# Optimization experiments

Hardware: AMD Instinct MI355X
Metric: run time of the kernel (lower is better)

The kernel has to match this reference:

```python
import jax, jax.numpy as jnp
import numpy as np

DIM = 1024          # config.dim
HID = 1024          # config.expert_hidden, already multiple of 64
N_EXP = 8           # num_routed_experts
TOP_K = 2           # top_k_experts
N_LOOPS = 4         # recursive_loops
B, S = 4, 1024


def setup_inputs() -> dict:
    key = jax.random.key(0)
    ks = jax.random.split(key, 10)
    def init(k, shape, fan_in):
        return jax.random.normal(k, shape, jnp.float32) * (fan_in ** -0.5)
    return {
        "x": jax.random.normal(ks[0], (B, S, DIM), jnp.float32),
        # shared expert (stored as [in, out] so forward is x @ W)
        "sg": init(ks[1], (DIM, HID), DIM),
        "su": init(ks[2], (DIM, HID), DIM),
        "sd": init(ks[3], (HID, DIM), HID),
        # routed experts stacked: [E, in, out]
        "Wg": init(ks[4], (N_EXP, DIM, HID), DIM),
        "Wu": init(ks[5], (N_EXP, DIM, HID), DIM),
        "Wd": init(ks[6], (N_EXP, HID, DIM), HID),
        # router: Linear(2*dim -> E, bias=False), stored [2*dim, E]
        "Wr": init(ks[7], (2 * DIM, N_EXP), 2 * DIM),
        # loop embedding table [num_loops, dim]
        "loop_table": jax.random.normal(ks[8], (N_LOOPS, DIM), jnp.float32),
        "loop_idx": 1,
    }


def _swiglu(x, wg, wu, wd):
    return (jax.nn.silu(x @ wg) * (x @ wu)) @ wd


def reference(x, sg, su, sd, Wg, Wu, Wd, Wr, loop_table, loop_idx):
    b, s, d = x.shape
    n = b * s
    xf = x.reshape(n, d)

    # shared expert (always active)
    shared = _swiglu(xf, sg, su, sd)  # [n, d]

    # loop-aware router: concat(x, loop_emb) @ Wr
    loop_emb = loop_table[loop_idx]                               # [d]
    router_in = jnp.concatenate(
        [xf, jnp.broadcast_to(loop_emb, (n, d))], axis=-1)        # [n, 2d]
    logits = router_in @ Wr                                       # [n, E]
    probs = jax.nn.sigmoid(logits)
    topw, topi = jax.lax.top_k(probs, TOP_K)                      # [n, k]

    # combine weights: combine[n, e] = sum_k topw[n,k] * (topi[n,k]==e)
    combine = jnp.zeros((n, N_EXP), x.dtype).at[
        jnp.arange(n)[:, None], topi].add(topw)                   # [n, E]

    # per-expert SwiGLU, combined with routing weights.
    # (dense-over-experts formulation; math identical to sort/dispatch/scatter)
    gate = jnp.einsum('nd,edh->neh', xf, Wg)                      # [n, E, H]
    up = jnp.einsum('nd,edh->neh', xf, Wu)                        # [n, E, H]
    h = jax.nn.silu(gate) * up                                    # [n, E, H]
    routed = jnp.einsum('neh,ehd,ne->nd', h, Wd, combine)         # [n, d]

    return (shared + routed).reshape(b, s, d)
```

## Files before the change

kernel.cpp:

```cpp
#include <hip/hip_runtime.h>
#include <cstdint>
#include <cstddef>

typedef __attribute__((ext_vector_type(8))) short short8;
typedef __attribute__((ext_vector_type(4))) float floatx4;

#define NTOK   4096
#define SHBASE 8192
#define NSLOT  12288
#define MAT_ELEMS (1024 * 1024)

__device__ __forceinline__ unsigned short f2b(float f) {
  unsigned u = __float_as_uint(f);
  u = (u + 0x7fffu + ((u >> 16) & 1u)) >> 16;
  return (unsigned short)u;
}

#define GLD16(gsrc, ldst)                                                              \
  __builtin_amdgcn_global_load_lds(                                                    \
      (const __attribute__((address_space(1))) unsigned int*)(gsrc),                   \
      (__attribute__((address_space(3))) unsigned int*)(ldst), 16, 0, 0)

__global__ void setup_kernel(const float* __restrict__ Wr,
                             const float* __restrict__ loopTable,
                             const int* __restrict__ loopIdx,
                             float* __restrict__ bias, int* __restrict__ cnt) {
  int t = threadIdx.x;
  if (t < 9) cnt[t] = (t == 8) ? NTOK : 0;
  if (t < 8) bias[t] = 0.0f;
  __syncthreads();
  const float* emb = loopTable + (size_t)(*loopIdx) * 1024;
  float partial[8] = {0, 0, 0, 0, 0, 0, 0, 0};
  for (int d = t; d < 1024; d += 256) {
    float ev = emb[d];
    const float* wr = Wr + (size_t)(1024 + d) * 8;
#pragma unroll
    for (int e = 0; e < 8; e++) partial[e] += ev * wr[e];
  }
#pragma unroll
  for (int off = 32; off > 0; off >>= 1)
#pragma unroll
    for (int e = 0; e < 8; e++) partial[e] += __shfl_xor(partial[e], off, 64);
  if ((t & 63) == 0)
#pragma unroll
    for (int e = 0; e < 8; e++) atomicAdd(&bias[e], partial[e]);
}

__global__ __launch_bounds__(256) void router_kernel(
    const float* __restrict__ x, const float* __restrict__ Wr,
    const float* __restrict__ bias, unsigned short* __restrict__ packedX,
    int* __restrict__ cnt, int* __restrict__ permSparse,
    float* __restrict__ wSparse, int* __restrict__ permToken,
    float* __restrict__ slotW) {
  int tid = threadIdx.x;
  int lane = tid & 63;
  int seg = __builtin_amdgcn_readfirstlane(tid >> 6);
  int tok0 = blockIdx.x << 6;
  int tok = tok0 + lane;

  __shared__ float red[4][64][9];
  __shared__ int lcnt[8];
  __shared__ int lbase[8];
  __shared__ int sE[64][2];
  __shared__ float sP[64][2];
  __shared__ int sPos[64][2];

  if (tid < 8) lcnt[tid] = 0;

  float lg[8] = {0, 0, 0, 0, 0, 0, 0, 0};
  const float* xr = x + (size_t)tok * 1024 + seg * 256;
  const float* wr = Wr + (size_t)seg * 256 * 8;
  for (int i = 0; i < 256; i += 4) {
    float4 xv = *(const float4*)(xr + i);
    float xs[4] = {xv.x, xv.y, xv.z, xv.w};
#pragma unroll
    for (int r = 0; r < 4; r++) {
      const float4* w4 = (const float4*)(wr + (size_t)(i + r) * 8);
      float4 wa = w4[0], wb = w4[1];
      float xv1 = xs[r];
      lg[0] += xv1 * wa.x; lg[1] += xv1 * wa.y; lg[2] += xv1 * wa.z; lg[3] += xv1 * wa.w;
      lg[4] += xv1 * wb.x; lg[5] += xv1 * wb.y; lg[6] += xv1 * wb.z; lg[7] += xv1 * wb.w;
    }
  }
#pragma unroll
  for (int e = 0; e < 8; e++) red[seg][lane][e] = lg[e];
  __syncthreads();

  if (tid < 64) {
    float l[8];
#pragma unroll
    for (int e = 0; e < 8; e++)
      l[e] = red[0][tid][e] + red[1][tid][e] + red[2][tid][e] + red[3][tid][e] + bias[e];
    int i0 = 0; float l0 = l[0];
#pragma unroll
    for (int e = 1; e < 8; e++) if (l[e] > l0) { l0 = l[e]; i0 = e; }
    int i1 = -1; float l1 = -1e30f;
#pragma unroll
    for (int e = 0; e < 8; e++) if (e != i0 && l[e] > l1) { l1 = l[e]; i1 = e; }
    float p0 = 1.0f / (1.0f + __expf(-l0));
    float p1 = 1.0f / (1.0f + __expf(-l1));
    sE[tid][0] = i0; sP[tid][0] = p0; sPos[tid][0] = atomicAdd(&lcnt[i0], 1);
    sE[tid][1] = i1; sP[tid][1] = p1; sPos[tid][1] = atomicAdd(&lcnt[i1], 1);
    int t = tok0 + tid;
    permToken[SHBASE + t] = t;
    slotW[SHBASE + t] = 1.0f;
  }
  __syncthreads();
  if (tid < 8) lbase[tid] = atomicAdd(&cnt[tid], lcnt[tid]);
  __syncthreads();
  if (tid < 64) {
    int t = tok0 + tid;
#pragma unroll
    for (int j = 0; j < 2; j++) {
      int e = sE[tid][j];
      int pos = lbase[e] + sPos[tid][j];
      permSparse[e * NTOK + pos] = t;
      wSparse[e * NTOK + pos] = sP[tid][j];
    }
  }

  const float4* xs4 = (const float4*)(x + (size_t)tok0 * 1024);
  uint2* dst = (uint2*)(packedX + (size_t)(SHBASE + tok0) * 1024);
  for (int i = tid; i < 64 * 256; i += 256) {
    float4 v = xs4[i];
    uint2 pk;
    pk.x = (unsigned)f2b(v.x) | ((unsigned)f2b(v.y) << 16);
    pk.y = (unsigned)f2b(v.z) | ((unsigned)f2b(v.w) << 16);
    dst[i] = pk;
  }
}

__global__ void scan_kernel(const int* __restrict__ cnt, int* __restrict__ offs) {
  if (threadIdx.x == 0) {
    int s = 0;
    for (int e = 0; e < 9; e++) { offs[e] = s; s += cnt[e]; }
  }
}

__global__ __launch_bounds__(256) void gather_kernel(
    const int* __restrict__ cnt, const int* __restrict__ offs,
    const int* __restrict__ permSparse, const float* __restrict__ wSparse,
    unsigned short* __restrict__ packedX, int* __restrict__ permToken,
    float* __restrict__ slotW) {
  int e = blockIdx.y;
  int r = (blockIdx.x << 2) + (threadIdx.x >> 6);
  int lane = threadIdx.x & 63;
  if (r >= cnt[e]) return;
  int token = permSparse[e * NTOK + r];
  int slot = offs[e] + r;
  if (lane == 0) { permToken[slot] = token; slotW[slot] = wSparse[e * NTOK + r]; }
  const uint4* s = (const uint4*)(packedX + (size_t)(SHBASE + token) * 1024) + lane * 2;
  uint4* d = (uint4*)(packedX + (size_t)slot * 1024) + lane * 2;
  uint4 a = s[0], b = s[1];
  d[0] = a; d[1] = b;
}

__global__ __launch_bounds__(256) void transpose_cast(
    const float* __restrict__ Wg, const float* __restrict__ Wu,
    const float* __restrict__ Wd, const float* __restrict__ sg,
    const float* __restrict__ su, const float* __restrict__ sd,
    unsigned short* __restrict__ Wt) {
  int m = blockIdx.z;
  int type = m / 9, e = m % 9;
  const float* src;
  if (type == 0)      src = (e < 8) ? Wg + (size_t)e * MAT_ELEMS : sg;
  else if (type == 1) src = (e < 8) ? Wu + (size_t)e * MAT_ELEMS : su;
  else                src = (e < 8) ? Wd + (size_t)e * MAT_ELEMS : sd;
  __shared__ float t[64][65];
  int bn = blockIdx.x << 6;
  int bk = blockIdx.y << 6;
  int tid = threadIdx.x;
  int ln = tid & 63, lk = tid >> 6;
#pragma unroll
  for (int i = 0; i < 16; i++) {
    int k = lk + (i << 2);
    t[k][ln] = src[(size_t)(bk + k) * 1024 + bn + ln];
  }
  __syncthreads();
  int wn = tid >> 4;
  int wk = (tid & 15) << 2;
  unsigned short* dstm = Wt + (size_t)m * MAT_ELEMS;
#pragma unroll
  for (int j = 0; j < 4; j++) {
    int n = wn + (j << 4);
    uint2 pk;
    pk.x = (unsigned)f2b(t[wk + 0][n]) | ((unsigned)f2b(t[wk + 1][n]) << 16);
    pk.y = (unsigned)f2b(t[wk + 2][n]) | ((unsigned)f2b(t[wk + 3][n]) << 16);
    *(uint2*)&dstm[(size_t)(bn + n) * 1024 + bk + wk] = pk;
  }
}

__global__ __launch_bounds__(256, 2) void gateup_gemm(
    const unsigned short* __restrict__ packedX, const unsigned short* __restrict__ Wt,
    const int* __restrict__ cnt, const int* __restrict__ offs,
    const float* __restrict__ slotW, unsigned short* __restrict__ Hbuf) {
  int e = blockIdx.z;
  int c = cnt[e];
  int m0 = blockIdx.y << 7;
  if (m0 >= c) return;
  int row_base = offs[e] + m0;
  int valid_m = c - m0; if (valid_m > 128) valid_m = 128;
  int n0 = blockIdx.x << 7;

  __shared__ unsigned short sA[128 * 64];
  __shared__ unsigned short sG[128 * 64];
  __shared__ unsigned short sU[128 * 64];

  int tid = threadIdx.x;
  int wv = tid >> 6, lane = tid & 63;
  int wm = wv >> 1, wn = wv & 1;

  const unsigned short* Ag = packedX + (size_t)row_base * 1024;
  const unsigned short* Gg = Wt + (size_t)e * MAT_ELEMS + (size_t)n0 * 1024;
  const unsigned short* Ug = Wt + (size_t)(9 + e) * MAT_ELEMS + (size_t)n0 * 1024;

  int srow = lane >> 3, schunk = lane & 7;

  floatx4 accG[4][4], accU[4][4];
#pragma unroll
  for (int i = 0; i < 4; i++)
#pragma unroll
    for (int j = 0; j < 4; j++) {
      accG[i][j] = floatx4{0.f, 0.f, 0.f, 0.f};
      accU[i][j] = floatx4{0.f, 0.f, 0.f, 0.f};
    }

  for (int kk = 0; kk < 1024; kk += 64) {
    __syncthreads();
#pragma unroll
    for (int j = 0; j < 4; j++) {
      int rb = (wv << 5) + (j << 3);
      size_t go = (size_t)(rb + srow) * 1024 + kk + (schunk << 3);
      GLD16(Ag + go, &sA[rb * 64]);
      GLD16(Gg + go, &sG[rb * 64]);
      GLD16(Ug + go, &sU[rb * 64]);
    }
    __syncthreads();
#pragma unroll
    for (int k0 = 0; k0 < 64; k0 += 32) {
      int aoff = ((lane >> 4) << 3) + k0;
      int arow = (wm << 6) + (lane & 15);
      short8 af[4];
#pragma unroll
      for (int mi = 0; mi < 4; mi++)
        af[mi] = *(const short8*)&sA[(arow + (mi << 4)) * 64 + aoff];
      int brow = (wn << 6) + (lane & 15);
#pragma unroll
      for (int ni = 0; ni < 4; ni++) {
        short8 gf = *(const short8*)&sG[(brow + (ni << 4)) * 64 + aoff];
        short8 uf = *(const short8*)&sU[(brow + (ni << 4)) * 64 + aoff];
#pragma unroll
        for (int mi = 0; mi < 4; mi++) {
          accG[mi][ni] = __builtin_amdgcn_mfma_f32_16x16x32_bf16(af[mi], gf, accG[mi][ni], 0, 0, 0);
          accU[mi][ni] = __builtin_amdgcn_mfma_f32_16x16x32_bf16(af[mi], uf, accU[mi][ni], 0, 0, 0);
        }
      }
    }
  }

  int colLane = lane & 15, quad = lane >> 4;
#pragma unroll
  for (int mi = 0; mi < 4; mi++) {
#pragma unroll
    for (int reg = 0; reg < 4; reg++) {
      int mrow = (wm << 6) + (mi << 4) + (quad << 2) + reg;
      if (mrow < valid_m) {
        int slot = row_base + mrow;
        float w = slotW[slot];
        unsigned short* hr = Hbuf + (size_t)slot * 1024 + n0 + (wn << 6) + colLane;
#pragma unroll
        for (int ni = 0; ni < 4; ni++) {
          float g = accG[mi][ni][reg];
          float u = accU[mi][ni][reg];
          float h = (g / (1.0f + __expf(-g))) * u * w;
          hr[ni << 4] = f2b(h);
        }
      }
    }
  }
}

template <bool ATOMIC>
__global__ __launch_bounds__(256, 2) void down_gemm(
    const unsigned short* __restrict__ Hbuf, const unsigned short* __restrict__ Wt,
    const int* __restrict__ cnt, const int* __restrict__ offs,
    const int* __restrict__ permToken, float* __restrict__ out, int e_base) {
  int e = e_base + blockIdx.z;
  int c = cnt[e];
  int m0 = blockIdx.y << 7;
  if (m0 >= c) return;
  int row_base = offs[e] + m0;
  int valid_m = c - m0; if (valid_m > 128) valid_m = 128;
  int n0 = blockIdx.x << 7;

  __shared__ unsigned short sA[128 * 64];
  __shared__ unsigned short sB[128 * 64];

  int tid = threadIdx.x;
  int wv = tid >> 6, lane = tid & 63;
  int wm = wv >> 1, wn = wv & 1;

  const unsigned short* Ag = Hbuf + (size_t)row_base * 1024;
  const unsigned short* Bg = Wt + (size_t)(18 + e) * MAT_ELEMS + (size_t)n0 * 1024;

  int srow = lane >> 3, schunk = lane & 7;

  floatx4 acc[4][4];
#pragma unroll
  for (int i = 0; i < 4; i++)
#pragma unroll
    for (int j = 0; j < 4; j++) acc[i][j] = floatx4{0.f, 0.f, 0.f, 0.f};

  for (int kk = 0; kk < 1024; kk += 64) {
    __syncthreads();
#pragma unroll
    for (int j = 0; j < 4; j++) {
      int rb = (wv << 5) + (j << 3);
      size_t go = (size_t)(rb + srow) * 1024 + kk + (schunk << 3);
      GLD16(Ag + go, &sA[rb * 64]);
      GLD16(Bg + go, &sB[rb * 64]);
    }
    __syncthreads();
#pragma unroll
    for (int k0 = 0; k0 < 64; k0 += 32) {
      int aoff = ((lane >> 4) << 3) + k0;
      int arow = (wm << 6) + (lane & 15);
      short8 af[4];
#pragma unroll
      for (int mi = 0; mi < 4; mi++)
        af[mi] = *(const short8*)&sA[(arow + (mi << 4)) * 64 + aoff];
      int brow = (wn << 6) + (lane & 15);
#pragma unroll
      for (int ni = 0; ni < 4; ni++) {
        short8 bf = *(const short8*)&sB[(brow + (ni << 4)) * 64 + aoff];
#pragma unroll
        for (int mi = 0; mi < 4; mi++)
          acc[mi][ni] = __builtin_amdgcn_mfma_f32_16x16x32_bf16(af[mi], bf, acc[mi][ni], 0, 0, 0);
      }
    }
  }

  int colLane = lane & 15, quad = lane >> 4;
#pragma unroll
  for (int mi = 0; mi < 4; mi++) {
#pragma unroll
    for (int reg = 0; reg < 4; reg++) {
      int mrow = (wm << 6) + (mi << 4) + (quad << 2) + reg;
      if (mrow < valid_m) {
        int slot = row_base + mrow;
        int token = permToken[slot];
        float* orow = out + (size_t)token * 1024 + n0 + (wn << 6) + colLane;
#pragma unroll
        for (int ni = 0; ni < 4; ni++) {
          float vvv = acc[mi][ni][reg];
          if (ATOMIC) atomicAdd(&orow[ni << 4], vvv);
          else        orow[ni << 4] = vvv;
        }
      }
    }
  }
}

extern "C" void kernel_launch(void* const* d_in, const int* in_sizes, int n_in,
                              void* d_out, int out_size, void* d_ws, size_t ws_size,
                              hipStream_t stream) {
  const float* x  = (const float*)d_in[0];
  const float* sg = (const float*)d_in[1];
  const float* su = (const float*)d_in[2];
  const float* sd = (const float*)d_in[3];
  const float* Wg = (const float*)d_in[4];
  const float* Wu = (const float*)d_in[5];
  const float* Wd = (const float*)d_in[6];
  const float* Wr = (const float*)d_in[7];
  const float* loopTable = (const float*)d_in[8];
  const int*   loopIdx   = (const int*)d_in[9];
  float* out = (float*)d_out;

  char* w = (char*)d_ws;
  unsigned short* Wt = (unsigned short*)w;       w += (size_t)27 * MAT_ELEMS * 2;
  unsigned short* packedX = (unsigned short*)w;  w += (size_t)NSLOT * 1024 * 2;
  unsigned short* Hbuf = (unsigned short*)w;     w += (size_t)NSLOT * 1024 * 2;
  int*   cnt        = (int*)w;   w += 16 * 4;
  int*   offs       = (int*)w;   w += 16 * 4;
  float* bias       = (float*)w; w += 16 * 4;
  int*   permSparse = (int*)w;   w += (size_t)8 * NTOK * 4;
  float* wSparse    = (float*)w; w += (size_t)8 * NTOK * 4;
  int*   permToken  = (int*)w;   w += (size_t)NSLOT * 4;
  float* slotW      = (float*)w; w += (size_t)NSLOT * 4;

  setup_kernel<<<1, 256, 0, stream>>>(Wr, loopTable, loopIdx, bias, cnt);
  router_kernel<<<64, 256, 0, stream>>>(x, Wr, bias, packedX, cnt, permSparse,
                                        wSparse, permToken, slotW);
  scan_kernel<<<1, 64, 0, stream>>>(cnt, offs);
  gather_kernel<<<dim3(1024, 8), 256, 0, stream>>>(cnt, offs, permSparse, wSparse,
                                                   packedX, permToken, slotW);
  transpose_cast<<<dim3(16, 16, 27), 256, 0, stream>>>(Wg, Wu, Wd, sg, su, sd, Wt);
  gateup_gemm<<<dim3(8, 32, 9), 256, 0, stream>>>(packedX, Wt, cnt, offs, slotW, Hbuf);
  down_gemm<false><<<dim3(8, 32, 1), 256, 0, stream>>>(Hbuf, Wt, cnt, offs, permToken, out, 8);
  down_gemm<true><<<dim3(8, 32, 8), 256, 0, stream>>>(Hbuf, Wt, cnt, offs, permToken, out, 0);
}
```

Measured before the change: 357.3 us.

## Gather token rows inside gate/up GEMM, swizzle LDS tiles, raise occupancy

The separate gather kernel that copied each routed token's bf16 row into a packed per-expert buffer is removed. The gate/up GEMM now loads A rows straight from the shared-token bf16 buffer through permToken indices, and a small finalize kernel only writes permToken and slotW. Both GEMMs also apply an XOR swizzle to the 16-byte chunk positions in LDS to cut bank conflicts on the MFMA fragment reads, and launch bounds go from 2 to 3 blocks per CU. The changes remove a full activation copy pass, but the indirect loads are less contiguous and the tighter register budget could cause spills.

```diff
diff --git a/kernel.cpp b/kernel.cpp
--- a/kernel.cpp
+++ b/kernel.cpp
@@ -137,22 +137,17 @@
   }
 }
 
-__global__ __launch_bounds__(256) void gather_kernel(
+__global__ __launch_bounds__(256) void finalize_kernel(
     const int* __restrict__ cnt, const int* __restrict__ offs,
     const int* __restrict__ permSparse, const float* __restrict__ wSparse,
-    unsigned short* __restrict__ packedX, int* __restrict__ permToken,
-    float* __restrict__ slotW) {
-  int e = blockIdx.y;
-  int r = (blockIdx.x << 2) + (threadIdx.x >> 6);
-  int lane = threadIdx.x & 63;
-  if (r >= cnt[e]) return;
-  int token = permSparse[e * NTOK + r];
-  int slot = offs[e] + r;
-  if (lane == 0) { permToken[slot] = token; slotW[slot] = wSparse[e * NTOK + r]; }
-  const uint4* s = (const uint4*)(packedX + (size_t)(SHBASE + token) * 1024) + lane * 2;
-  uint4* d = (uint4*)(packedX + (size_t)slot * 1024) + lane * 2;
-  uint4 a = s[0], b = s[1];
-  d[0] = a; d[1] = b;
+    int* __restrict__ permToken, float* __restrict__ slotW) {
+  int idx = blockIdx.x * 256 + threadIdx.x;
+  int e = idx >> 12, r = idx & (NTOK - 1);
+  if (e < 8 && r < cnt[e]) {
+    int slot = offs[e] + r;
+    permToken[slot] = permSparse[e * NTOK + r];
+    slotW[slot] = wSparse[e * NTOK + r];
+  }
 }
 
 __global__ __launch_bounds__(256) void transpose_cast(
@@ -190,10 +185,11 @@
   }
 }
 
-__global__ __launch_bounds__(256, 2) void gateup_gemm(
-    const unsigned short* __restrict__ packedX, const unsigned short* __restrict__ Wt,
+__global__ __launch_bounds__(256, 3) void gateup_gemm(
+    const unsigned short* __restrict__ Xb, const unsigned short* __restrict__ Wt,
     const int* __restrict__ cnt, const int* __restrict__ offs,
-    const float* __restrict__ slotW, unsigned short* __restrict__ Hbuf) {
+    const int* __restrict__ permToken, const float* __restrict__ slotW,
+    unsigned short* __restrict__ Hbuf) {
   int e = blockIdx.z;
   int c = cnt[e];
   int m0 = blockIdx.y << 7;
@@ -210,11 +206,16 @@
   int wv = tid >> 6, lane = tid & 63;
   int wm = wv >> 1, wn = wv & 1;
 
-  const unsigned short* Ag = packedX + (size_t)row_base * 1024;
   const unsigned short* Gg = Wt + (size_t)e * MAT_ELEMS + (size_t)n0 * 1024;
   const unsigned short* Ug = Wt + (size_t)(9 + e) * MAT_ELEMS + (size_t)n0 * 1024;
 
   int srow = lane >> 3, schunk = lane & 7;
+  int swc = (schunk ^ srow) << 3;
+
+  int myTok[4];
+#pragma unroll
+  for (int j = 0; j < 4; j++)
+    myTok[j] = permToken[row_base + (wv << 5) + (j << 3) + srow];
 
   floatx4 accG[4][4], accU[4][4];
 #pragma unroll
@@ -230,25 +231,25 @@
 #pragma unroll
     for (int j = 0; j < 4; j++) {
       int rb = (wv << 5) + (j << 3);
-      size_t go = (size_t)(rb + srow) * 1024 + kk + (schunk << 3);
-      GLD16(Ag + go, &sA[rb * 64]);
-      GLD16(Gg + go, &sG[rb * 64]);
-      GLD16(Ug + go, &sU[rb * 64]);
+      size_t gw = (size_t)(rb + srow) * 1024 + kk + swc;
+      GLD16(Xb + (size_t)myTok[j] * 1024 + kk + swc, &sA[rb * 64]);
+      GLD16(Gg + gw, &sG[rb * 64]);
+      GLD16(Ug + gw, &sU[rb * 64]);
     }
     __syncthreads();
 #pragma unroll
     for (int k0 = 0; k0 < 64; k0 += 32) {
-      int aoff = ((lane >> 4) << 3) + k0;
+      int swoff = (((lane >> 4) + (k0 >> 3)) ^ (lane & 7)) << 3;
       int arow = (wm << 6) + (lane & 15);
       short8 af[4];
 #pragma unroll
       for (int mi = 0; mi < 4; mi++)
-        af[mi] = *(const short8*)&sA[(arow + (mi << 4)) * 64 + aoff];
+        af[mi] = *(const short8*)&sA[(arow + (mi << 4)) * 64 + swoff];
       int brow = (wn << 6) + (lane & 15);
 #pragma unroll
       for (int ni = 0; ni < 4; ni++) {
-        short8 gf = *(const short8*)&sG[(brow + (ni << 4)) * 64 + aoff];
-        short8 uf = *(const short8*)&sU[(brow + (ni << 4)) * 64 + aoff];
+        short8 gf = *(const short8*)&sG[(brow + (ni << 4)) * 64 + swoff];
+        short8 uf = *(const short8*)&sU[(brow + (ni << 4)) * 64 + swoff];
 #pragma unroll
         for (int mi = 0; mi < 4; mi++) {
           accG[mi][ni] = __builtin_amdgcn_mfma_f32_16x16x32_bf16(af[mi], gf, accG[mi][ni], 0, 0, 0);
@@ -281,7 +282,7 @@
 }
 
 template <bool ATOMIC>
-__global__ __launch_bounds__(256, 2) void down_gemm(
+__global__ __launch_bounds__(256, 3) void down_gemm(
     const unsigned short* __restrict__ Hbuf, const unsigned short* __restrict__ Wt,
     const int* __restrict__ cnt, const int* __restrict__ offs,
     const int* __restrict__ permToken, float* __restrict__ out, int e_base) {
@@ -304,6 +305,7 @@
   const unsigned short* Bg = Wt + (size_t)(18 + e) * MAT_ELEMS + (size_t)n0 * 1024;
 
   int srow = lane >> 3, schunk = lane & 7;
+  int swc = (schunk ^ srow) << 3;
 
   floatx4 acc[4][4];
 #pragma unroll
@@ -316,23 +318,23 @@
 #pragma unroll
     for (int j = 0; j < 4; j++) {
       int rb = (wv << 5) + (j << 3);
-      size_t go = (size_t)(rb + srow) * 1024 + kk + (schunk << 3);
-      GLD16(Ag + go, &sA[rb * 64]);
-      GLD16(Bg + go, &sB[rb * 64]);
+      size_t gw = (size_t)(rb + srow) * 1024 + kk + swc;
+      GLD16(Ag + gw, &sA[rb * 64]);
+      GLD16(Bg + gw, &sB[rb * 64]);
     }
     __syncthreads();
 #pragma unroll
     for (int k0 = 0; k0 < 64; k0 += 32) {
-      int aoff = ((lane >> 4) << 3) + k0;
+      int swoff = (((lane >> 4) + (k0 >> 3)) ^ (lane & 7)) << 3;
       int arow = (wm << 6) + (lane & 15);
       short8 af[4];
 #pragma unroll
       for (int mi = 0; mi < 4; mi++)
-        af[mi] = *(const short8*)&sA[(arow + (mi << 4)) * 64 + aoff];
+        af[mi] = *(const short8*)&sA[(arow + (mi << 4)) * 64 + swoff];
       int brow = (wn << 6) + (lane & 15);
 #pragma unroll
       for (int ni = 0; ni < 4; ni++) {
-        short8 bf = *(const short8*)&sB[(brow + (ni << 4)) * 64 + aoff];
+        short8 bf = *(const short8*)&sB[(brow + (ni << 4)) * 64 + swoff];
 #pragma unroll
         for (int mi = 0; mi < 4; mi++)
           acc[mi][ni] = __builtin_amdgcn_mfma_f32_16x16x32_bf16(af[mi], bf, acc[mi][ni], 0, 0, 0);
@@ -388,14 +390,17 @@
   int*   permToken  = (int*)w;   w += (size_t)NSLOT * 4;
   float* slotW      = (float*)w; w += (size_t)NSLOT * 4;
 
+  unsigned short* Xb = packedX + (size_t)SHBASE * 1024;
+
   setup_kernel<<<1, 256, 0, stream>>>(Wr, loopTable, loopIdx, bias, cnt);
   router_kernel<<<64, 256, 0, stream>>>(x, Wr, bias, packedX, cnt, permSparse,
                                         wSparse, permToken, slotW);
   scan_kernel<<<1, 64, 0, stream>>>(cnt, offs);
-  gather_kernel<<<dim3(1024, 8), 256, 0, stream>>>(cnt, offs, permSparse, wSparse,
-                                                   packedX, permToken, slotW);
+  finalize_kernel<<<128, 256, 0, stream>>>(cnt, offs, permSparse, wSparse,
+                                           permToken, slotW);
   transpose_cast<<<dim3(16, 16, 27), 256, 0, stream>>>(Wg, Wu, Wd, sg, su, sd, Wt);
-  gateup_gemm<<<dim3(8, 32, 9), 256, 0, stream>>>(packedX, Wt, cnt, offs, slotW, Hbuf);
+  gateup_gemm<<<dim3(8, 32, 9), 256, 0, stream>>>(Xb, Wt, cnt, offs, permToken,
+                                                  slotW, Hbuf);
   down_gemm<false><<<dim3(8, 32, 1), 256, 0, stream>>>(Hbuf, Wt, cnt, offs, permToken, out, 8);
   down_gemm<true><<<dim3(8, 32, 8), 256, 0, stream>>>(Hbuf, Wt, cnt, offs, permToken, out, 0);
 }
```

Result: slower. 404.9 us (+13.3%).
